# Kernel optimization log

Hardware: AMD Instinct MI355X
Metric: run time of the kernel (lower is better)

## Reference

```python
import jax, jax.numpy as jnp
import numpy as np

N = 10000      # total nodes
E = 320000     # total edges (avg degree 32)
T = 8          # time steps
F = 32         # feature width (in = hidden = out)
L = 3          # len(hidden_sizes) + 1 layers
EPS = 1e-5     # BatchNorm eps


def setup_inputs() -> dict:
    key = jax.random.key(0)
    ks = jax.random.split(key, 6)
    node_features = jax.random.normal(ks[0], (N, F), dtype=jnp.float32)
    edges_weight = jax.random.uniform(ks[1], (T, E), dtype=jnp.float32)
    src = jax.random.randint(ks[2], (E,), 0, N, dtype=jnp.int32)
    dst = jax.random.randint(ks[3], (E,), 0, N, dtype=jnp.int32)
    Ws = jax.random.normal(ks[4], (L, F, F), dtype=jnp.float32) / np.float32(np.sqrt(F))
    bs = jnp.zeros((L, F), dtype=jnp.float32)
    gammas = jnp.ones((L, F), dtype=jnp.float32)
    betas = jnp.zeros((L, F), dtype=jnp.float32)
    return dict(node_features=node_features, edges_weight=edges_weight,
                src=src, dst=dst, Ws=Ws, bs=bs, gammas=gammas, betas=betas)


def reference(node_features, edges_weight, src, dst, Ws, bs, gammas, betas):
    w_et = edges_weight.T            # (E, T), matches edge_weights.t()
    n = node_features.shape[0]
    h = node_features                # (N, F) first layer, (N, T, F) after
    for l in range(L):
        hs = h[src]                  # gather source-node features
        if hs.ndim == 2:
            hs = hs[:, None, :]      # (E, 1, F) -> broadcast over T
        msg = hs * w_et[:, :, None]  # u_mul_e: (E, T, F)
        agg = jax.ops.segment_sum(msg, dst, num_segments=n)  # sum per dst: (N, T, F)
        out = jnp.einsum('ntf,of->nto', agg, Ws[l]) + bs[l]  # Linear
        # BatchNorm1d (training mode): stats over (N, T) per channel, biased var
        mean = out.mean(axis=(0, 1))
        var = out.var(axis=(0, 1))
        out = (out - mean) * jax.lax.rsqrt(var + EPS) * gammas[l] + betas[l]
        h = jax.nn.relu(out)
    return h                         # (N, T, F)
```

## Files before the change

### kernel.cpp

```cpp
#include <hip/hip_runtime.h>

#define TF 8
#define FD 32
#define WS 33
#define EPSV 1e-5f

__device__ __forceinline__ void atomAddF(float* p, float v) {
#if defined(__HIP_PLATFORM_AMD__)
    unsafeAtomicAdd(p, v);
#else
    atomicAdd(p, v);
#endif
}

__device__ __forceinline__ unsigned int f2bfu(float x) {
    unsigned int u = __float_as_uint(x);
    return (u + 0x7FFFu + ((u >> 16) & 1u)) >> 16;
}
__device__ __forceinline__ float bfx(unsigned int w, int hi) {
    return __uint_as_float(hi ? (w & 0xFFFF0000u) : (w << 16));
}

__global__ __launch_bounds__(256) void hist_kernel(
    const int* __restrict__ dst, int* __restrict__ counts, int E)
{
    int e = blockIdx.x * 256 + threadIdx.x;
    if (e < E) atomicAdd(&counts[dst[e]], 1);
}

__global__ __launch_bounds__(1024) void scan_kernel(
    const int* __restrict__ counts, int* __restrict__ rowptr,
    int* __restrict__ cursor, int Nn)
{
    __shared__ int totals[1024];
    int tid = threadIdx.x;
    int per = (Nn + 1023) >> 10;
    int start = tid * per;
    int end = min(start + per, Nn);
    if (end < start) end = start;
    int s = 0;
    for (int i = start; i < end; ++i) s += counts[i];
    totals[tid] = s;
    __syncthreads();
    for (int off = 1; off < 1024; off <<= 1) {
        int t2 = (tid >= off) ? totals[tid - off] : 0;
        __syncthreads();
        totals[tid] += t2;
        __syncthreads();
    }
    int running = totals[tid] - s;
    for (int i = start; i < end; ++i) {
        rowptr[i] = running;
        cursor[i] = running;
        running += counts[i];
    }
    if (tid == 1023) rowptr[Nn] = totals[1023];
}

__global__ __launch_bounds__(256) void fillA_kernel(
    const int* __restrict__ src, const int* __restrict__ dst,
    const float* __restrict__ w, int* __restrict__ cursor,
    int* __restrict__ ssrc, uint4* __restrict__ wsb, int E)
{
    int e = blockIdx.x * 256 + threadIdx.x;
    if (e >= E) return;
    int d = dst[e];
    int j = atomicAdd(&cursor[d], 1);
    ssrc[j] = src[e];
    uint4 p;
    p.x = f2bfu(w[(size_t)0 * E + e]) | (f2bfu(w[(size_t)1 * E + e]) << 16);
    p.y = f2bfu(w[(size_t)2 * E + e]) | (f2bfu(w[(size_t)3 * E + e]) << 16);
    p.z = f2bfu(w[(size_t)4 * E + e]) | (f2bfu(w[(size_t)5 * E + e]) << 16);
    p.w = f2bfu(w[(size_t)6 * E + e]) | (f2bfu(w[(size_t)7 * E + e]) << 16);
    wsb[j] = p;
}

template <int MODE, int OUTB>
__global__ __launch_bounds__(256) void agg_gemm6_kernel(
    const float* __restrict__ hf, const uint4* __restrict__ hb,
    const float* __restrict__ coefIn,
    const int* __restrict__ rowptr, const int* __restrict__ ssrc,
    const uint4* __restrict__ wsb,
    const float* __restrict__ W, const float* __restrict__ bias,
    unsigned int* __restrict__ outU, float* __restrict__ outF,
    float* __restrict__ stats)
{
    __shared__ float Wt[FD * WS];
    __shared__ float red[512];
    __shared__ float pacc[8 * TF * FD];
    int tid = threadIdx.x;
    int slot = tid >> 5, f = tid & 31;
    {
        int ff = tid & 31;
        Wt[ff * WS + (tid >> 5)] = W[tid];
        Wt[ff * WS + ((tid + 256) >> 5)] = W[tid + 256];
        Wt[ff * WS + ((tid + 512) >> 5)] = W[tid + 512];
        Wt[ff * WS + ((tid + 768) >> 5)] = W[tid + 768];
    }
    float cA = 0.f, cB = 0.f;
    if (MODE == 1) { cA = coefIn[f]; cB = coefIn[FD + f]; }

    int node = blockIdx.x;
    int rs = rowptr[node], re = rowptr[node + 1];

    float acc[TF];
    #pragma unroll
    for (int t = 0; t < TF; ++t) acc[t] = 0.f;

    int j = rs + slot;
    if (j < re) {
        int s0 = ssrc[j];
        int j1 = j + 8;
        int s1 = (j1 < re) ? ssrc[j1] : 0;
        uint4 wp = wsb[j];
        float  hf0 = 0.f; uint4 hp0 = {0u,0u,0u,0u};
        if (MODE == 0) hf0 = hf[(size_t)s0 * FD + f];
        else           hp0 = hb[(size_t)s0 * FD + f];

        for (; j < re; j += 8, j1 += 8) {
            int j2 = j1 + 8;
            int s2 = (j2 < re) ? ssrc[j2] : 0;
            uint4 wp_n = {0u,0u,0u,0u};
            if (j1 < re) wp_n = wsb[j1];
            float hf_n = 0.f; uint4 hp_n = {0u,0u,0u,0u};
            if (MODE == 0) hf_n = hf[(size_t)s1 * FD + f];
            else           hp_n = hb[(size_t)s1 * FD + f];

            unsigned int ww[4] = { wp.x, wp.y, wp.z, wp.w };
            if (MODE == 0) {
                #pragma unroll
                for (int t = 0; t < TF; ++t)
                    acc[t] = fmaf(bfx(ww[t >> 1], t & 1), hf0, acc[t]);
            } else {
                unsigned int hw[4] = { hp0.x, hp0.y, hp0.z, hp0.w };
                #pragma unroll
                for (int t = 0; t < TF; ++t) {
                    float hr = bfx(hw[t >> 1], t & 1);
                    float hn = fmaxf(0.f, fmaf(hr, cA, cB));
                    acc[t] = fmaf(bfx(ww[t >> 1], t & 1), hn, acc[t]);
                }
            }
            s1 = s2; wp = wp_n; hf0 = hf_n; hp0 = hp_n;
        }
    }

    #pragma unroll
    for (int t = 0; t < TF; ++t)
        pacc[slot * (TF * FD) + t * FD + f] = acc[t];
    __syncthreads();
    int t2 = tid >> 5;
    float asum = 0.f;
    #pragma unroll
    for (int sl = 0; sl < 8; ++sl)
        asum += pacc[sl * (TF * FD) + t2 * FD + f];
    red[tid] = asum;
    __syncthreads();

    float oval = bias[f];
    #pragma unroll
    for (int k = 0; k < FD; ++k)
        oval = fmaf(red[t2 * FD + k], Wt[k * WS + f], oval);
    if (!OUTB)
        outF[(size_t)node * (TF * FD) + tid] = oval;

    __syncthreads();
    red[tid] = oval;
    red[256 + tid] = oval * oval;
    __syncthreads();
    if (OUTB) {
        if (tid < 128) {
            int ff = tid >> 2, q = tid & 3;
            unsigned int lo = f2bfu(red[(q * 2) * FD + ff]);
            unsigned int hi = f2bfu(red[(q * 2 + 1) * FD + ff]);
            outU[(size_t)node * 128 + ff * 4 + q] = lo | (hi << 16);
        }
        __syncthreads();
    }
    #pragma unroll
    for (int stride = 128; stride >= 32; stride >>= 1) {
        if (tid < stride) {
            red[tid] += red[tid + stride];
            red[256 + tid] += red[256 + tid + stride];
        }
        __syncthreads();
    }
    if (tid < 32) {
        int slot2 = blockIdx.x & 31;
        atomAddF(&stats[slot2 * 64 + tid], red[tid]);
        atomAddF(&stats[slot2 * 64 + 32 + tid], red[256 + tid]);
    }
}

__global__ void finalize_kernel(const float* __restrict__ stats,
                                const float* __restrict__ gamma,
                                const float* __restrict__ beta,
                                float* __restrict__ coef, float inv_count)
{
    int o = threadIdx.x;
    float s = 0.f, sq = 0.f;
    #pragma unroll
    for (int k = 0; k < 32; ++k) { s += stats[k * 64 + o]; sq += stats[k * 64 + 32 + o]; }
    float mean = s * inv_count;
    float var  = sq * inv_count - mean * mean;
    float sc   = gamma[o] * rsqrtf(var + EPSV);
    coef[o]      = sc;
    coef[FD + o] = beta[o] - mean * sc;
}

__global__ __launch_bounds__(256) void norm_relu_kernel(
    float* __restrict__ x, const float* __restrict__ coef, int n4)
{
    int gid = blockIdx.x * 256 + threadIdx.x;
    if (gid >= n4) return;
    float4 v = ((const float4*)x)[gid];
    int o = (gid * 4) & 31;
    float4 r;
    r.x = fmaxf(0.f, fmaf(v.x, coef[o],     coef[32 + o]));
    r.y = fmaxf(0.f, fmaf(v.y, coef[o + 1], coef[33 + o]));
    r.z = fmaxf(0.f, fmaf(v.z, coef[o + 2], coef[34 + o]));
    r.w = fmaxf(0.f, fmaf(v.w, coef[o + 3], coef[35 + o]));
    ((float4*)x)[gid] = r;
}

__global__ __launch_bounds__(256) void scatter0_kernel(
    const float* __restrict__ h, const float* __restrict__ w,
    const int* __restrict__ src, const int* __restrict__ dst,
    float* __restrict__ agg, int E)
{
    int gid = blockIdx.x * 256 + threadIdx.x;
    int e = gid >> 5;
    if (e >= E) return;
    int f = gid & 31;
    int s = src[e], d = dst[e];
    float hv = h[(size_t)s * FD + f];
    float* aggd = agg + (size_t)d * (TF * FD) + f;
    #pragma unroll
    for (int t = 0; t < TF; ++t)
        atomAddF(aggd + t * FD, w[(size_t)t * E + e] * hv);
}

__global__ __launch_bounds__(256) void scatterL_kernel(
    const float* __restrict__ h, const float* __restrict__ w,
    const int* __restrict__ src, const int* __restrict__ dst,
    float* __restrict__ agg, int E)
{
    int gid = blockIdx.x * 256 + threadIdx.x;
    int e = gid >> 5;
    if (e >= E) return;
    int f = gid & 31;
    int s = src[e], d = dst[e];
    const float* hs = h + (size_t)s * (TF * FD) + f;
    float* aggd = agg + (size_t)d * (TF * FD) + f;
    #pragma unroll
    for (int t = 0; t < TF; ++t)
        atomAddF(aggd + t * FD, w[(size_t)t * E + e] * hs[t * FD]);
}

__global__ __launch_bounds__(256) void gemm_stats_kernel(
    const float* __restrict__ agg, const float* __restrict__ W,
    const float* __restrict__ bias, float* __restrict__ out,
    float* __restrict__ stats, int nrows)
{
    __shared__ float Wt[FD * FD];
    __shared__ float rows[8 * FD];
    int tid = threadIdx.x;
    for (int i = tid; i < FD * FD; i += 256) {
        int o = i >> 5, f = i & 31;
        Wt[f * FD + o] = W[i];
    }
    int o = tid & 31;
    int r = tid >> 5;
    float b = bias[o];
    float sum = 0.f, sumsq = 0.f;
    int ngroups = (nrows + 7) >> 3;
    for (int g = blockIdx.x; g < ngroups; g += gridDim.x) {
        int row0 = g * 8;
        __syncthreads();
        int idx = row0 * FD + tid;
        rows[tid] = (idx < nrows * FD) ? agg[idx] : 0.f;
        __syncthreads();
        int row = row0 + r;
        if (row < nrows) {
            float acc = b;
            #pragma unroll
            for (int f2 = 0; f2 < FD; ++f2)
                acc = fmaf(rows[r * FD + f2], Wt[f2 * FD + o], acc);
            out[(size_t)row * FD + o] = acc;
            sum += acc;
            sumsq += acc * acc;
        }
    }
    __syncthreads();
    rows[tid] = sum;
    Wt[tid] = sumsq;
    __syncthreads();
    for (int stride = 128; stride >= 32; stride >>= 1) {
        if (tid < stride) { rows[tid] += rows[tid + stride]; Wt[tid] += Wt[tid + stride]; }
        __syncthreads();
    }
    if (tid < 32) {
        int slot = blockIdx.x & 31;
        atomAddF(&stats[slot * 64 + tid], rows[tid]);
        atomAddF(&stats[slot * 64 + 32 + tid], Wt[tid]);
    }
}

extern "C" void kernel_launch(void* const* d_in, const int* in_sizes, int n_in,
                              void* d_out, int out_size, void* d_ws, size_t ws_size,
                              hipStream_t stream)
{
    const float* nf  = (const float*)d_in[0];
    const float* wgt = (const float*)d_in[1];
    const int*   src = (const int*)d_in[2];
    const int*   dst = (const int*)d_in[3];
    const float* Ws  = (const float*)d_in[4];
    const float* bs  = (const float*)d_in[5];
    const float* gam = (const float*)d_in[6];
    const float* bet = (const float*)d_in[7];

    int E  = in_sizes[2];
    int Nn = in_sizes[0] / FD;
    int nrows = Nn * TF;
    int n4 = nrows * FD / 4;
    float inv_count = 1.0f / (float)nrows;
    float* out = (float*)d_out;

    size_t offCounts = 0;
    size_t offStats  = offCounts + (size_t)Nn;
    size_t offCoef   = offStats + 3 * 2048;
    size_t offCursor = offCoef + 3 * 64;
    size_t offRowptr = offCursor + (size_t)Nn;
    size_t offSsrc   = offRowptr + (size_t)Nn + 4;
    size_t offWsb    = (offSsrc + (size_t)E + 3) & ~(size_t)3;
    size_t offHb0    = offWsb + 4 * (size_t)E;
    size_t offHb1    = offHb0 + 128 * (size_t)Nn;
    size_t needW     = (offHb1 + 128 * (size_t)Nn) * 4;

    int eb = (E + 255) / 256;

    if (ws_size >= needW) {
        int*          base   = (int*)d_ws;
        int*          counts = base + offCounts;
        float*        stats  = (float*)(base + offStats);
        float*        coef   = (float*)(base + offCoef);
        int*          cursor = base + offCursor;
        int*          rowptr = base + offRowptr;
        int*          ssrc   = base + offSsrc;
        uint4*        wsb    = (uint4*)(base + offWsb);
        unsigned int* hb0    = (unsigned int*)(base + offHb0);
        unsigned int* hb1    = (unsigned int*)(base + offHb1);

        hipMemsetAsync(counts, 0, ((size_t)Nn + 3 * 2048) * sizeof(int), stream);
        hist_kernel<<<eb, 256, 0, stream>>>(dst, counts, E);
        scan_kernel<<<1, 1024, 0, stream>>>(counts, rowptr, cursor, Nn);
        fillA_kernel<<<eb, 256, 0, stream>>>(src, dst, wgt, cursor, ssrc, wsb, E);

        agg_gemm6_kernel<0, 1><<<Nn, 256, 0, stream>>>(
            nf, nullptr, nullptr, rowptr, ssrc, wsb, Ws, bs,
            hb0, nullptr, stats);
        finalize_kernel<<<1, 32, 0, stream>>>(stats, gam, bet, coef, inv_count);
        agg_gemm6_kernel<1, 1><<<Nn, 256, 0, stream>>>(
            nullptr, (const uint4*)hb0, coef, rowptr, ssrc, wsb,
            Ws + FD * FD, bs + FD, hb1, nullptr, stats + 2048);
        finalize_kernel<<<1, 32, 0, stream>>>(
            stats + 2048, gam + FD, bet + FD, coef + 64, inv_count);
        agg_gemm6_kernel<1, 0><<<Nn, 256, 0, stream>>>(
            nullptr, (const uint4*)hb1, coef + 64, rowptr, ssrc, wsb,
            Ws + 2 * FD * FD, bs + 2 * FD, nullptr, out, stats + 2 * 2048);
        finalize_kernel<<<1, 32, 0, stream>>>(
            stats + 2 * 2048, gam + 2 * FD, bet + 2 * FD, coef + 2 * 64, inv_count);
        norm_relu_kernel<<<(n4 + 255) / 256, 256, 0, stream>>>(out, coef + 2 * 64, n4);
    } else {
        float* agg   = (float*)d_ws;
        float* stats = agg + (size_t)nrows * FD;
        float* coef  = stats + 2048;
        int scatterBlocks = (E * 32 + 255) / 256;
        for (int l = 0; l < 3; ++l) {
            hipMemsetAsync(agg, 0, (size_t)nrows * FD * sizeof(float), stream);
            hipMemsetAsync(stats, 0, 2048 * sizeof(float), stream);
            if (l == 0)
                scatter0_kernel<<<scatterBlocks, 256, 0, stream>>>(nf, wgt, src, dst, agg, E);
            else
                scatterL_kernel<<<scatterBlocks, 256, 0, stream>>>(out, wgt, src, dst, agg, E);
            gemm_stats_kernel<<<2048, 256, 0, stream>>>(
                agg, Ws + l * FD * FD, bs + l * FD, out, stats, nrows);
            finalize_kernel<<<1, 32, 0, stream>>>(
                stats, gam + l * FD, bet + l * FD, coef, inv_count);
            norm_relu_kernel<<<(n4 + 255) / 256, 256, 0, stream>>>(out, coef, n4);
        }
    }
}
```

Measured before the change: 219.9 us.

## Process four nodes per block and accumulate BN stats in registers

Each block of the aggregate+GEMM kernel now loops over four destination nodes instead of one. The shared-memory load of the weight matrix and the atomic stats flush are paid once per four nodes. BatchNorm sum and sum-of-squares are kept in registers and reduced once at the end with wave shuffles. The bf16 output packing now uses a cross-lane shuffle instead of a shared-memory round trip. The trade-off is a quarter as many blocks, so fewer blocks are in flight to hide gather latency, and nodes inside a block run one after another.

```diff
diff --git a/kernel.cpp b/kernel.cpp
--- a/kernel.cpp
+++ b/kernel.cpp
@@ -3,6 +3,7 @@
 #define TF 8
 #define FD 32
 #define WS 33
+#define NPB 4
 #define EPSV 1e-5f
 
 __device__ __forceinline__ void atomAddF(float* p, float v) {
@@ -76,17 +77,17 @@
 }
 
 template <int MODE, int OUTB>
-__global__ __launch_bounds__(256) void agg_gemm6_kernel(
+__global__ __launch_bounds__(256) void agg_gemm7_kernel(
     const float* __restrict__ hf, const uint4* __restrict__ hb,
     const float* __restrict__ coefIn,
     const int* __restrict__ rowptr, const int* __restrict__ ssrc,
     const uint4* __restrict__ wsb,
     const float* __restrict__ W, const float* __restrict__ bias,
     unsigned int* __restrict__ outU, float* __restrict__ outF,
-    float* __restrict__ stats)
+    float* __restrict__ stats, int Nn)
 {
     __shared__ float Wt[FD * WS];
-    __shared__ float red[512];
+    __shared__ float red[256];
     __shared__ float pacc[8 * TF * FD];
     int tid = threadIdx.x;
     int slot = tid >> 5, f = tid & 31;
@@ -99,95 +100,105 @@
     }
     float cA = 0.f, cB = 0.f;
     if (MODE == 1) { cA = coefIn[f]; cB = coefIn[FD + f]; }
-
-    int node = blockIdx.x;
-    int rs = rowptr[node], re = rowptr[node + 1];
-
-    float acc[TF];
-    #pragma unroll
-    for (int t = 0; t < TF; ++t) acc[t] = 0.f;
-
-    int j = rs + slot;
-    if (j < re) {
-        int s0 = ssrc[j];
-        int j1 = j + 8;
-        int s1 = (j1 < re) ? ssrc[j1] : 0;
-        uint4 wp = wsb[j];
-        float  hf0 = 0.f; uint4 hp0 = {0u,0u,0u,0u};
-        if (MODE == 0) hf0 = hf[(size_t)s0 * FD + f];
-        else           hp0 = hb[(size_t)s0 * FD + f];
-
-        for (; j < re; j += 8, j1 += 8) {
-            int j2 = j1 + 8;
-            int s2 = (j2 < re) ? ssrc[j2] : 0;
-            uint4 wp_n = {0u,0u,0u,0u};
-            if (j1 < re) wp_n = wsb[j1];
-            float hf_n = 0.f; uint4 hp_n = {0u,0u,0u,0u};
-            if (MODE == 0) hf_n = hf[(size_t)s1 * FD + f];
-            else           hp_n = hb[(size_t)s1 * FD + f];
-
-            unsigned int ww[4] = { wp.x, wp.y, wp.z, wp.w };
-            if (MODE == 0) {
-                #pragma unroll
-                for (int t = 0; t < TF; ++t)
-                    acc[t] = fmaf(bfx(ww[t >> 1], t & 1), hf0, acc[t]);
-            } else {
-                unsigned int hw[4] = { hp0.x, hp0.y, hp0.z, hp0.w };
-                #pragma unroll
-                for (int t = 0; t < TF; ++t) {
-                    float hr = bfx(hw[t >> 1], t & 1);
-                    float hn = fmaxf(0.f, fmaf(hr, cA, cB));
-                    acc[t] = fmaf(bfx(ww[t >> 1], t & 1), hn, acc[t]);
+    float bia = bias[f];
+    int t2 = tid >> 5;
+    float ssum = 0.f, ssq = 0.f;
+
+    for (int ni = 0; ni < NPB; ++ni) {
+        int node = blockIdx.x * NPB + ni;
+        if (node >= Nn) break;
+        int rs = rowptr[node], re = rowptr[node + 1];
+
+        float acc[TF];
+        #pragma unroll
+        for (int t = 0; t < TF; ++t) acc[t] = 0.f;
+
+        int j = rs + slot;
+        if (j < re) {
+            int s0 = ssrc[j];
+            int j1 = j + 8;
+            int s1 = (j1 < re) ? ssrc[j1] : 0;
+            uint4 wp = wsb[j];
+            float  hf0 = 0.f; uint4 hp0 = {0u,0u,0u,0u};
+            if (MODE == 0) hf0 = hf[(size_t)s0 * FD + f];
+            else           hp0 = hb[(size_t)s0 * FD + f];
+
+            for (; j < re; j += 8, j1 += 8) {
+                int j2 = j1 + 8;
+                int s2 = (j2 < re) ? ssrc[j2] : 0;
+                uint4 wp_n = {0u,0u,0u,0u};
+                if (j1 < re) wp_n = wsb[j1];
+                float hf_n = 0.f; uint4 hp_n = {0u,0u,0u,0u};
+                if (MODE == 0) hf_n = hf[(size_t)s1 * FD + f];
+                else           hp_n = hb[(size_t)s1 * FD + f];
+
+                unsigned int ww[4] = { wp.x, wp.y, wp.z, wp.w };
+                if (MODE == 0) {
+                    #pragma unroll
+                    for (int t = 0; t < TF; ++t)
+                        acc[t] = fmaf(bfx(ww[t >> 1], t & 1), hf0, acc[t]);
+                } else {
+                    unsigned int hw[4] = { hp0.x, hp0.y, hp0.z, hp0.w };
+                    #pragma unroll
+                    for (int t = 0; t < TF; ++t) {
+                        float hr = bfx(hw[t >> 1], t & 1);
+                        float hn = fmaxf(0.f, fmaf(hr, cA, cB));
+                        acc[t] = fmaf(bfx(ww[t >> 1], t & 1), hn, acc[t]);
+                    }
                 }
+                s1 = s2; wp = wp_n; hf0 = hf_n; hp0 = hp_n;
             }
-            s1 = s2; wp = wp_n; hf0 = hf_n; hp0 = hp_n;
         }
-    }
-
-    #pragma unroll
-    for (int t = 0; t < TF; ++t)
-        pacc[slot * (TF * FD) + t * FD + f] = acc[t];
+
+        #pragma unroll
+        for (int t = 0; t < TF; ++t)
+            pacc[slot * (TF * FD) + t * FD + f] = acc[t];
+        __syncthreads();
+        float asum = 0.f;
+        #pragma unroll
+        for (int sl = 0; sl < 8; ++sl)
+            asum += pacc[sl * (TF * FD) + t2 * FD + f];
+        red[tid] = asum;
+        __syncthreads();
+
+        float oval = bia;
+        #pragma unroll
+        for (int k = 0; k < FD; ++k)
+            oval = fmaf(red[t2 * FD + k], Wt[k * WS + f], oval);
+
+        if (!OUTB) {
+            outF[(size_t)node * (TF * FD) + tid] = oval;
+        } else {
+            float pv = __shfl_xor(oval, 32);
+            if ((tid & 63) < 32) {
+                unsigned int lo = f2bfu(oval), hi = f2bfu(pv);
+                int w = tid >> 6;
+                outU[(size_t)node * 128 + f * 4 + w] = lo | (hi << 16);
+            }
+        }
+        ssum += oval;
+        ssq  += oval * oval;
+        __syncthreads();
+    }
+
+    ssum += __shfl_xor(ssum, 32);
+    ssq  += __shfl_xor(ssq, 32);
+    int w = tid >> 6;
+    if ((tid & 63) < 32) {
+        red[w * 32 + f]  = ssum;
+        pacc[w * 32 + f] = ssq;
+    }
     __syncthreads();
-    int t2 = tid >> 5;
-    float asum = 0.f;
-    #pragma unroll
-    for (int sl = 0; sl < 8; ++sl)
-        asum += pacc[sl * (TF * FD) + t2 * FD + f];
-    red[tid] = asum;
-    __syncthreads();
-
-    float oval = bias[f];
-    #pragma unroll
-    for (int k = 0; k < FD; ++k)
-        oval = fmaf(red[t2 * FD + k], Wt[k * WS + f], oval);
-    if (!OUTB)
-        outF[(size_t)node * (TF * FD) + tid] = oval;
-
-    __syncthreads();
-    red[tid] = oval;
-    red[256 + tid] = oval * oval;
-    __syncthreads();
-    if (OUTB) {
-        if (tid < 128) {
-            int ff = tid >> 2, q = tid & 3;
-            unsigned int lo = f2bfu(red[(q * 2) * FD + ff]);
-            unsigned int hi = f2bfu(red[(q * 2 + 1) * FD + ff]);
-            outU[(size_t)node * 128 + ff * 4 + q] = lo | (hi << 16);
+    if (tid < 32) {
+        float s = 0.f, q = 0.f;
+        #pragma unroll
+        for (int k = 0; k < 4; ++k) {
+            s += red[k * 32 + tid];
+            q += pacc[k * 32 + tid];
         }
-        __syncthreads();
-    }
-    #pragma unroll
-    for (int stride = 128; stride >= 32; stride >>= 1) {
-        if (tid < stride) {
-            red[tid] += red[tid + stride];
-            red[256 + tid] += red[256 + tid + stride];
-        }
-        __syncthreads();
-    }
-    if (tid < 32) {
         int slot2 = blockIdx.x & 31;
-        atomAddF(&stats[slot2 * 64 + tid], red[tid]);
-        atomAddF(&stats[slot2 * 64 + 32 + tid], red[256 + tid]);
+        atomAddF(&stats[slot2 * 64 + tid], s);
+        atomAddF(&stats[slot2 * 64 + 32 + tid], q);
     }
 }
 
@@ -337,6 +348,7 @@
     size_t needW     = (offHb1 + 128 * (size_t)Nn) * 4;
 
     int eb = (E + 255) / 256;
+    int nb = (Nn + NPB - 1) / NPB;
 
     if (ws_size >= needW) {
         int*          base   = (int*)d_ws;
@@ -355,18 +367,18 @@
         scan_kernel<<<1, 1024, 0, stream>>>(counts, rowptr, cursor, Nn);
         fillA_kernel<<<eb, 256, 0, stream>>>(src, dst, wgt, cursor, ssrc, wsb, E);
 
-        agg_gemm6_kernel<0, 1><<<Nn, 256, 0, stream>>>(
+        agg_gemm7_kernel<0, 1><<<nb, 256, 0, stream>>>(
             nf, nullptr, nullptr, rowptr, ssrc, wsb, Ws, bs,
-            hb0, nullptr, stats);
+            hb0, nullptr, stats, Nn);
         finalize_kernel<<<1, 32, 0, stream>>>(stats, gam, bet, coef, inv_count);
-        agg_gemm6_kernel<1, 1><<<Nn, 256, 0, stream>>>(
+        agg_gemm7_kernel<1, 1><<<nb, 256, 0, stream>>>(
             nullptr, (const uint4*)hb0, coef, rowptr, ssrc, wsb,
-            Ws + FD * FD, bs + FD, hb1, nullptr, stats + 2048);
+            Ws + FD * FD, bs + FD, hb1, nullptr, stats + 2048, Nn);
         finalize_kernel<<<1, 32, 0, stream>>>(
             stats + 2048, gam + FD, bet + FD, coef + 64, inv_count);
-        agg_gemm6_kernel<1, 0><<<Nn, 256, 0, stream>>>(
+        agg_gemm7_kernel<1, 0><<<nb, 256, 0, stream>>>(
             nullptr, (const uint4*)hb1, coef + 64, rowptr, ssrc, wsb,
-            Ws + 2 * FD * FD, bs + 2 * FD, nullptr, out, stats + 2 * 2048);
+            Ws + 2 * FD * FD, bs + 2 * FD, nullptr, out, stats + 2 * 2048, Nn);
         finalize_kernel<<<1, 32, 0, stream>>>(
             stats + 2 * 2048, gam + 2 * FD, bet + 2 * FD, coef + 2 * 64, inv_count);
         norm_relu_kernel<<<(n4 + 255) / 256, 256, 0, stream>>>(out, coef + 2 * 64, n4);
```

After: 229.0 us. 1.04x slower.
